# Kernel optimization log

Measured on AMD Instinct MI355X. Metric: run time of the kernel, lower is better.

The kernel has to match this reference:

```python
import jax, jax.numpy as jnp
import numpy as np

B, L, D = 256, 512, 768
ATTN_H, WIDTH_DIM = 1000, 20
BINS = jnp.array([1, 2, 3, 4, 5, 6, 7, 8, 12, 16, 20, 24, 32, 64, 128], dtype=jnp.int64)


def setup_inputs() -> dict:
    key = jax.random.key(0)
    ks = jax.random.split(key, 20)
    s = 0.02
    embeds = jax.random.normal(ks[0], (B, L, D), dtype=jnp.float32)
    spans = jnp.sort(jax.random.randint(ks[1], (B, 2), 0, L, dtype=jnp.int64), axis=1)
    inp = {
        "embeds": embeds,
        "spans": spans,
        # attention scorer: Linear(768,1000) -> LeakyReLU -> Linear(1000,1)
        "aw1": jax.random.normal(ks[2], (D, ATTN_H), dtype=jnp.float32) * s,
        "ab1": jnp.zeros((ATTN_H,), dtype=jnp.float32),
        "aw2": jax.random.normal(ks[3], (ATTN_H, 1), dtype=jnp.float32) * s,
        "ab2": jnp.zeros((1,), dtype=jnp.float32),
        # width embedding: [len(bins)+1 = 16, 20]
        "width_emb": jax.random.normal(ks[4], (16, WIDTH_DIM), dtype=jnp.float32) * s,
        # score MLP: 2324 -> 1024 -> 512 -> 256 -> 30
        "sw1": jax.random.normal(ks[5], (2324, 1024), dtype=jnp.float32) * s,
        "sb1": jnp.zeros((1024,), dtype=jnp.float32),
        "sw2": jax.random.normal(ks[6], (1024, 512), dtype=jnp.float32) * s,
        "sb2": jnp.zeros((512,), dtype=jnp.float32),
        "sw3": jax.random.normal(ks[7], (512, 256), dtype=jnp.float32) * s,
        "sb3": jnp.zeros((256,), dtype=jnp.float32),
        "sw4": jax.random.normal(ks[8], (256, 30), dtype=jnp.float32) * s,
        "sb4": jnp.zeros((30,), dtype=jnp.float32),
    }
    return inp


def reference(embeds, spans, aw1, ab1, aw2, ab2, width_emb,
              sw1, sb1, sw2, sb2, sw3, sb3, sw4, sb4):
    b, l, d = embeds.shape
    start, end = spans[:, 0], spans[:, 1]

    # gather start/end token embeds -> [B, 2*D]
    se = jnp.take_along_axis(embeds, spans[:, :, None], axis=1).reshape(b, 2 * d)

    # attention logits over all tokens: Linear -> LeakyReLU -> Linear
    h = jax.nn.leaky_relu(embeds @ aw1 + ab1)          # [B, L, 1000]
    attns = (h @ aw2 + ab2)[..., 0]                     # [B, L]

    # ragged per-span softmax pooling, vectorized via masking (inclusive span)
    cols = jnp.arange(l, dtype=spans.dtype)[None, :]
    mask = (cols >= start[:, None]) & (cols <= end[:, None])
    w = jax.nn.softmax(jnp.where(mask, attns, jnp.float32(-1e30)), axis=1)
    w = w * mask.astype(w.dtype)
    attn_embeds = jnp.einsum("bl,bld->bd", w, embeds)   # [B, D]

    # width bucket embedding
    widths = end - start + 1
    idx = jnp.sum(widths[:, None] > BINS[None, :], axis=1)
    wemb = width_emb[idx]                                # [B, 20]

    x = jnp.concatenate([se, attn_embeds, wemb], axis=1)  # [B, 2324]
    x = jax.nn.leaky_relu(x @ sw1 + sb1)
    x = jax.nn.leaky_relu(x @ sw2 + sb2)
    x = jax.nn.leaky_relu(x @ sw3 + sb3)
    return x @ sw4 + sb4                                  # [B, 30]
```

## Files before the change

### kernel.cpp

```cpp
#include <hip/hip_runtime.h>
#include <hip/hip_bf16.h>

#define B_   256
#define L_   512
#define D_   768
#define H_   1000
#define NPAD 1024
#define XDIM 2324
#define MAXPOS (B_*L_)

typedef _Float16 half8 __attribute__((ext_vector_type(8)));
typedef float    f32x4 __attribute__((ext_vector_type(4)));

__global__ __launch_bounds__(256) void scan_kernel(const int* __restrict__ spans,
                                                   int* __restrict__ meta) {
    int b = threadIdx.x;
    int s = spans[2 * b], e = spans[2 * b + 1];
    s = min(max(s, 0), L_ - 1);
    e = min(max(e, s), L_ - 1);
    int w = e - s + 1;
    __shared__ int sw[256];
    sw[b] = w;
    __syncthreads();
    for (int d = 1; d < 256; d <<= 1) {
        int v = 0;
        if (b >= d) v = sw[b - d];
        __syncthreads();
        if (b >= d) sw[b] += v;
        __syncthreads();
    }
    meta[b]       = sw[b] - w;
    meta[256 + b] = s;
    meta[512 + b] = e;
    if (b == 255) meta[768] = sw[255];
}

__global__ __launch_bounds__(256) void pos_fill(const int* __restrict__ meta,
                                                int* __restrict__ pos_list) {
    int b = blockIdx.x;
    int off = meta[b], start = meta[256 + b], end = meta[512 + b];
    int w = end - start + 1;
    for (int i = threadIdx.x; i < w; i += blockDim.x)
        pos_list[off + i] = (b << 16) | (start + i);
}

__global__ __launch_bounds__(256) void transpose_w(const float* __restrict__ aw1,
                                                   _Float16* __restrict__ WbT) {
    int k0 = blockIdx.x * 32, n0 = blockIdx.y * 32;
    int tx = threadIdx.x & 31, ty = threadIdx.x >> 5;
    __shared__ float T[32][33];
#pragma unroll
    for (int it = 0; it < 4; it++) {
        int k = k0 + ty + 8 * it;
        int n = n0 + tx;
        T[ty + 8 * it][tx] = (n < H_) ? aw1[(size_t)k * H_ + n] : 0.f;
    }
    __syncthreads();
#pragma unroll
    for (int it = 0; it < 4; it++) {
        int n = n0 + ty + 8 * it;
        WbT[(size_t)n * D_ + k0 + tx] = (_Float16)T[tx][ty + 8 * it];
    }
}

#define AP 776
__global__ __launch_bounds__(256) void attn_gemm_v2(
    const float* __restrict__ embeds, const _Float16* __restrict__ WbT,
    const float* __restrict__ ab1, const float* __restrict__ aw2,
    const int* __restrict__ pos_list, const int* __restrict__ meta,
    float* __restrict__ attns) {
    int npos = meta[768];
    int m0 = blockIdx.x * 32;
    if (m0 >= npos) return;
    int t = threadIdx.x;
    int lane = t & 63, w = t >> 6;
    int q = lane >> 4, l15 = lane & 15;

    __shared__ alignas(16) _Float16 As[32][AP];
    __shared__ unsigned rowoff[32];
    __shared__ float attns_s[4][32];

    if (t < 32) {
        unsigned off = 0;
        int m = m0 + t;
        if (m < npos) {
            int p = pos_list[m];
            off = (unsigned)((p >> 16) * (L_ * D_) + (p & 0xffff) * D_);
        }
        rowoff[t] = off;
    }
    __syncthreads();

    {
        int row = t >> 3;
        int cs = (t & 7) * 96;
        const float* src = embeds + rowoff[row] + cs;
#pragma unroll
        for (int i2 = 0; i2 < 12; i2++) {
            float4 v0 = *(const float4*)(src + i2 * 8);
            float4 v1 = *(const float4*)(src + i2 * 8 + 4);
            half8 h;
            h[0] = (_Float16)v0.x; h[1] = (_Float16)v0.y;
            h[2] = (_Float16)v0.z; h[3] = (_Float16)v0.w;
            h[4] = (_Float16)v1.x; h[5] = (_Float16)v1.y;
            h[6] = (_Float16)v1.z; h[7] = (_Float16)v1.w;
            *(half8*)&As[row][cs + i2 * 8] = h;
        }
    }
    __syncthreads();

    float pacc[2][4];
#pragma unroll
    for (int i = 0; i < 2; i++)
#pragma unroll
        for (int r = 0; r < 4; r++) pacc[i][r] = 0.f;

    for (int g = 0; g < 4; g++) {
        int colbase = w * 256 + g * 64;
        const _Float16* bbase = WbT + (size_t)(colbase + l15) * D_ + q * 8;
        f32x4 acc[2][4];
#pragma unroll
        for (int i = 0; i < 2; i++)
#pragma unroll
            for (int j = 0; j < 4; j++) acc[i][j] = (f32x4){0.f, 0.f, 0.f, 0.f};

        for (int k0 = 0; k0 < D_; k0 += 32) {
            half8 bf[4];
#pragma unroll
            for (int j = 0; j < 4; j++)
                bf[j] = *(const half8*)(bbase + (size_t)j * 16 * D_ + k0);
            half8 af[2];
#pragma unroll
            for (int i = 0; i < 2; i++)
                af[i] = *(const half8*)&As[l15 + 16 * i][k0 + q * 8];
#pragma unroll
            for (int i = 0; i < 2; i++)
#pragma unroll
                for (int j = 0; j < 4; j++)
                    acc[i][j] = __builtin_amdgcn_mfma_f32_16x16x32_f16(af[i], bf[j], acc[i][j], 0, 0, 0);
        }

        float bj[4], aj[4];
#pragma unroll
        for (int j = 0; j < 4; j++) {
            int col = colbase + j * 16 + l15;
            bool v = col < H_;
            bj[j] = v ? ab1[col] : 0.f;
            aj[j] = v ? aw2[col] : 0.f;
        }
#pragma unroll
        for (int i = 0; i < 2; i++) {
#pragma unroll
            for (int r = 0; r < 4; r++) {
                float p = 0.f;
#pragma unroll
                for (int j = 0; j < 4; j++) {
                    float h = acc[i][j][r] + bj[j];
                    h = h > 0.f ? h : 0.01f * h;
                    p += h * aj[j];
                }
                p += __shfl_xor(p, 1);
                p += __shfl_xor(p, 2);
                p += __shfl_xor(p, 4);
                p += __shfl_xor(p, 8);
                pacc[i][r] += p;
            }
        }
    }
    if (l15 == 0) {
#pragma unroll
        for (int i = 0; i < 2; i++)
#pragma unroll
            for (int r = 0; r < 4; r++)
                attns_s[w][i * 16 + q * 4 + r] = pacc[i][r];
    }
    __syncthreads();
    if (t < 32 && m0 + t < npos)
        attns[m0 + t] = attns_s[0][t] + attns_s[1][t] + attns_s[2][t] + attns_s[3][t];
}

__global__ __launch_bounds__(256) void build_x(
    const float* __restrict__ embeds, const float* __restrict__ attns,
    const int* __restrict__ meta, const float* __restrict__ width_emb,
    float* __restrict__ x) {
    int b = blockIdx.x, s = blockIdx.y, t = threadIdx.x;
    int off = meta[b], start = meta[256 + b], end = meta[512 + b];
    int w = end - start + 1;
    __shared__ float sv[512];
    __shared__ float red[256];
    for (int i = t; i < w; i += 256) sv[i] = attns[off + i];
    __syncthreads();
    float m = -3.0e38f;
    for (int i = t; i < w; i += 256) m = fmaxf(m, sv[i]);
    red[t] = m;
    __syncthreads();
    for (int st = 128; st > 0; st >>= 1) {
        if (t < st) red[t] = fmaxf(red[t], red[t + st]);
        __syncthreads();
    }
    float mx = red[0];
    __syncthreads();
    float ssum = 0.f;
    for (int i = t; i < w; i += 256) {
        float e = __expf(sv[i] - mx);
        sv[i] = e;
        ssum += e;
    }
    red[t] = ssum;
    __syncthreads();
    for (int st = 128; st > 0; st >>= 1) {
        if (t < st) red[t] += red[t + st];
        __syncthreads();
    }
    float inv = 1.0f / red[0];
    __syncthreads();

    int dim = s * 256 + t;
    const float* base = embeds + ((size_t)b * L_ + start) * D_ + dim;
    float acc = 0.f;
    int i = 0;
    for (; i + 3 < w; i += 4) {
        float w0 = sv[i], w1 = sv[i + 1], w2 = sv[i + 2], w3 = sv[i + 3];
        const float* p = base + (size_t)i * D_;
        acc += w0 * p[0] + w1 * p[D_] + w2 * p[2 * D_] + w3 * p[3 * D_];
    }
    for (; i < w; i++) acc += sv[i] * base[(size_t)i * D_];

    float* xb = x + (size_t)b * XDIM;
    xb[1536 + dim] = acc * inv;
    xb[dim]        = base[0];
    xb[768 + dim]  = embeds[((size_t)b * L_ + end) * D_ + dim];
    if (s == 0 && t < 20) {
        const int bins[15] = {1, 2, 3, 4, 5, 6, 7, 8, 12, 16, 20, 24, 32, 64, 128};
        int idx = 0;
#pragma unroll
        for (int q2 = 0; q2 < 15; q2++) idx += (w > bins[q2]);
        xb[2304 + t] = width_emb[idx * 20 + t];
    }
}

__global__ __launch_bounds__(256) void mlp_gemm_sk(
    const float* __restrict__ A, const float* __restrict__ W,
    float* __restrict__ out, int M, int N, int K, int kchunk) {
    __shared__ float As[16][68];
    __shared__ float Ws[16][64];
    int t = threadIdx.x;
    int tx = t & 15, ty = t >> 4;
    int m0 = blockIdx.x * 64, n0 = blockIdx.y * 64;
    int ks = blockIdx.z * kchunk;
    int ke = min(ks + kchunk, K);
    if (ks >= ke) return;
    int ar = t >> 2, akc = (t & 3) * 4;
    int wk = t >> 4, wnc = (t & 15) * 4;
    bool n4 = ((N & 3) == 0);

    float acc[4][4];
#pragma unroll
    for (int i = 0; i < 4; i++)
#pragma unroll
        for (int j = 0; j < 4; j++) acc[i][j] = 0.f;

    auto loadA = [&](int k0) -> float4 {
        float4 r = make_float4(0.f, 0.f, 0.f, 0.f);
        int k = k0 + akc;
        if (k < ke) r = *(const float4*)(A + (size_t)(m0 + ar) * K + k);
        return r;
    };
    auto loadW = [&](int k0) -> float4 {
        float4 r = make_float4(0.f, 0.f, 0.f, 0.f);
        int k = k0 + wk;
        if (k < ke) {
            int n = n0 + wnc;
            const float* p = W + (size_t)k * N + n;
            if (n4) {
                r = *(const float4*)p;
            } else {
                float tmp[4];
#pragma unroll
                for (int q2 = 0; q2 < 4; q2++)
                    tmp[q2] = (n + q2 < N) ? p[q2] : 0.f;
                r = make_float4(tmp[0], tmp[1], tmp[2], tmp[3]);
            }
        }
        return r;
    };

    float4 aR = loadA(ks), wR = loadW(ks);
    for (int k0 = ks; k0 < ke; k0 += 16) {
        As[akc + 0][ar] = aR.x;
        As[akc + 1][ar] = aR.y;
        As[akc + 2][ar] = aR.z;
        As[akc + 3][ar] = aR.w;
        *(float4*)&Ws[wk][wnc] = wR;
        __syncthreads();
        if (k0 + 16 < ke) { aR = loadA(k0 + 16); wR = loadW(k0 + 16); }
#pragma unroll
        for (int kk = 0; kk < 16; kk++) {
            float4 a = *(const float4*)&As[kk][ty * 4];
            float4 b = *(const float4*)&Ws[kk][tx * 4];
            float av[4] = {a.x, a.y, a.z, a.w};
            float bv[4] = {b.x, b.y, b.z, b.w};
#pragma unroll
            for (int i = 0; i < 4; i++)
#pragma unroll
                for (int j = 0; j < 4; j++) acc[i][j] += av[i] * bv[j];
        }
        __syncthreads();
    }
#pragma unroll
    for (int i = 0; i < 4; i++) {
#pragma unroll
        for (int j = 0; j < 4; j++) {
            int nn = n0 + tx * 4 + j;
            if (nn < N)
                atomicAdd(&out[(size_t)(m0 + ty * 4 + i) * N + nn], acc[i][j]);
        }
    }
}

__global__ __launch_bounds__(256) void bias_act(
    const float* __restrict__ src, const float* __restrict__ bias,
    float* __restrict__ dst, int total, int N, int leaky) {
    int i = blockIdx.x * 256 + threadIdx.x;
    int stride = gridDim.x * 256;
    for (; i < total; i += stride) {
        float v = src[i] + bias[i % N];
        if (leaky) v = v > 0.f ? v : 0.01f * v;
        dst[i] = v;
    }
}

extern "C" void kernel_launch(void* const* d_in, const int* in_sizes, int n_in,
                              void* d_out, int out_size, void* d_ws, size_t ws_size,
                              hipStream_t stream) {
    const float* embeds    = (const float*)d_in[0];
    const int*   spans     = (const int*)d_in[1];
    const float* aw1       = (const float*)d_in[2];
    const float* ab1       = (const float*)d_in[3];
    const float* aw2       = (const float*)d_in[4];
    const float* width_emb = (const float*)d_in[6];
    const float* sw1 = (const float*)d_in[7],  *sb1 = (const float*)d_in[8];
    const float* sw2 = (const float*)d_in[9],  *sb2 = (const float*)d_in[10];
    const float* sw3 = (const float*)d_in[11], *sb3 = (const float*)d_in[12];
    const float* sw4 = (const float*)d_in[13], *sb4 = (const float*)d_in[14];
    float* out = (float*)d_out;

    char* ws = (char*)d_ws;
    float*     attns    = (float*)ws;
    int*       pos_list = (int*)(ws + (size_t)MAXPOS * 4);
    int*       meta     = (int*)(ws + (size_t)MAXPOS * 8);
    _Float16*  WbT      = (_Float16*)(ws + (size_t)MAXPOS * 8 + 4096);
    float* x  = (float*)(ws + (size_t)MAXPOS * 8 + 4096 + (size_t)NPAD * D_ * 2);
    float* y1 = x + (size_t)B_ * XDIM;
    float* y2 = y1 + (size_t)B_ * 1024;
    float* y3 = y2 + (size_t)B_ * 512;
    float* y4 = y3 + (size_t)B_ * 256;
    size_t ybytes = ((size_t)B_ * (1024 + 512 + 256 + 30)) * 4;

    hipMemsetAsync(y1, 0, ybytes, stream);
    scan_kernel<<<1, 256, 0, stream>>>(spans, meta);
    pos_fill<<<B_, 256, 0, stream>>>(meta, pos_list);
    transpose_w<<<dim3(D_ / 32, NPAD / 32), 256, 0, stream>>>(aw1, WbT);
    attn_gemm_v2<<<MAXPOS / 32, 256, 0, stream>>>(
        embeds, WbT, ab1, aw2, pos_list, meta, attns);
    build_x<<<dim3(B_, 3), 256, 0, stream>>>(embeds, attns, meta, width_emb, x);

    mlp_gemm_sk<<<dim3(4, 16, 8), 256, 0, stream>>>(x,  sw1, y1, B_, 1024, XDIM, 292);
    bias_act<<<256, 256, 0, stream>>>(y1, sb1, y1, B_ * 1024, 1024, 1);
    mlp_gemm_sk<<<dim3(4, 8, 8), 256, 0, stream>>>(y1, sw2, y2, B_, 512, 1024, 128);
    bias_act<<<128, 256, 0, stream>>>(y2, sb2, y2, B_ * 512, 512, 1);
    mlp_gemm_sk<<<dim3(4, 4, 8), 256, 0, stream>>>(y2, sw3, y3, B_, 256, 512, 64);
    bias_act<<<64, 256, 0, stream>>>(y3, sb3, y3, B_ * 256, 256, 1);
    mlp_gemm_sk<<<dim3(4, 1, 8), 256, 0, stream>>>(y3, sw4, y4, B_, 30, 256, 32);
    bias_act<<<30, 256, 0, stream>>>(y4, sb4, out, B_ * 30, 30, 0);
}
```

Measured before the change: 903.7 us.

## Pre-pack attention weights into MFMA fragment layout and double-buffer B loads

Replaces the weight transpose with a packing kernel that writes aw1 in the exact per-lane MFMA fragment order, so each wave's B loads become fully contiguous 16-byte-per-lane reads. The attention GEMM inner loop now double-buffers the B fragments across k-chunks to overlap global loads with MFMA work. The span pooling loop is unrolled to eight independent accumulators to raise memory-level parallelism. The packing kernel's reads of aw1 are strided and uncoalesced, which may cost more than the old transpose, and the extra accumulators slightly change floating-point summation order.

Result: slower. 937.1 us (+3.7%).

```diff
diff --git a/kernel.cpp b/kernel.cpp
--- a/kernel.cpp
+++ b/kernel.cpp
@@ -8,6 +8,7 @@
 #define NPAD 1024
 #define XDIM 2324
 #define MAXPOS (B_*L_)
+#define NKC  24
 
 typedef _Float16 half8 __attribute__((ext_vector_type(8)));
 typedef float    f32x4 __attribute__((ext_vector_type(4)));
@@ -44,28 +45,24 @@
         pos_list[off + i] = (b << 16) | (start + i);
 }
 
-__global__ __launch_bounds__(256) void transpose_w(const float* __restrict__ aw1,
-                                                   _Float16* __restrict__ WbT) {
-    int k0 = blockIdx.x * 32, n0 = blockIdx.y * 32;
-    int tx = threadIdx.x & 31, ty = threadIdx.x >> 5;
-    __shared__ float T[32][33];
-#pragma unroll
-    for (int it = 0; it < 4; it++) {
-        int k = k0 + ty + 8 * it;
-        int n = n0 + tx;
-        T[ty + 8 * it][tx] = (n < H_) ? aw1[(size_t)k * H_ + n] : 0.f;
-    }
-    __syncthreads();
-#pragma unroll
-    for (int it = 0; it < 4; it++) {
-        int n = n0 + ty + 8 * it;
-        WbT[(size_t)n * D_ + k0 + tx] = (_Float16)T[tx][ty + 8 * it];
-    }
+__global__ __launch_bounds__(64) void pack_b(const float* __restrict__ aw1,
+                                             _Float16* __restrict__ Bp) {
+    int gi = blockIdx.x, kc = blockIdx.y;
+    int l = threadIdx.x;
+    int col = gi * 16 + (l & 15);
+    int kbase = kc * 32 + (l >> 4) * 8;
+    half8 h;
+#pragma unroll
+    for (int e = 0; e < 8; e++) {
+        float v = (col < H_) ? aw1[(size_t)(kbase + e) * H_ + col] : 0.f;
+        h[e] = (_Float16)v;
+    }
+    *(half8*)&Bp[(((size_t)gi * NKC + kc) * 64 + l) * 8] = h;
 }
 
 #define AP 776
 __global__ __launch_bounds__(256) void attn_gemm_v2(
-    const float* __restrict__ embeds, const _Float16* __restrict__ WbT,
+    const float* __restrict__ embeds, const _Float16* __restrict__ Bp,
     const float* __restrict__ ab1, const float* __restrict__ aw2,
     const int* __restrict__ pos_list, const int* __restrict__ meta,
     float* __restrict__ attns) {
@@ -117,27 +114,50 @@
 
     for (int g = 0; g < 4; g++) {
         int colbase = w * 256 + g * 64;
-        const _Float16* bbase = WbT + (size_t)(colbase + l15) * D_ + q * 8;
+        int gi0 = colbase >> 4;
+        const _Float16* bb = Bp + ((size_t)gi0 * NKC * 64) * 8 + (size_t)lane * 8;
         f32x4 acc[2][4];
 #pragma unroll
         for (int i = 0; i < 2; i++)
 #pragma unroll
             for (int j = 0; j < 4; j++) acc[i][j] = (f32x4){0.f, 0.f, 0.f, 0.f};
 
-        for (int k0 = 0; k0 < D_; k0 += 32) {
-            half8 bf[4];
+        half8 bfA[4], bfB[4];
+#pragma unroll
+        for (int j = 0; j < 4; j++)
+            bfA[j] = *(const half8*)(bb + (size_t)j * (NKC * 64 * 8));
+
+        for (int kc = 0; kc < NKC; kc += 2) {
 #pragma unroll
             for (int j = 0; j < 4; j++)
-                bf[j] = *(const half8*)(bbase + (size_t)j * 16 * D_ + k0);
-            half8 af[2];
-#pragma unroll
-            for (int i = 0; i < 2; i++)
-                af[i] = *(const half8*)&As[l15 + 16 * i][k0 + q * 8];
-#pragma unroll
-            for (int i = 0; i < 2; i++)
+                bfB[j] = *(const half8*)(bb + (size_t)j * (NKC * 64 * 8) + (size_t)(kc + 1) * 512);
+            {
+                half8 af[2];
+#pragma unroll
+                for (int i = 0; i < 2; i++)
+                    af[i] = *(const half8*)&As[l15 + 16 * i][kc * 32 + q * 8];
+#pragma unroll
+                for (int i = 0; i < 2; i++)
+#pragma unroll
+                    for (int j = 0; j < 4; j++)
+                        acc[i][j] = __builtin_amdgcn_mfma_f32_16x16x32_f16(af[i], bfA[j], acc[i][j], 0, 0, 0);
+            }
+            if (kc + 2 < NKC) {
 #pragma unroll
                 for (int j = 0; j < 4; j++)
-                    acc[i][j] = __builtin_amdgcn_mfma_f32_16x16x32_f16(af[i], bf[j], acc[i][j], 0, 0, 0);
+                    bfA[j] = *(const half8*)(bb + (size_t)j * (NKC * 64 * 8) + (size_t)(kc + 2) * 512);
+            }
+            {
+                half8 af[2];
+#pragma unroll
+                for (int i = 0; i < 2; i++)
+                    af[i] = *(const half8*)&As[l15 + 16 * i][(kc + 1) * 32 + q * 8];
+#pragma unroll
+                for (int i = 0; i < 2; i++)
+#pragma unroll
+                    for (int j = 0; j < 4; j++)
+                        acc[i][j] = __builtin_amdgcn_mfma_f32_16x16x32_f16(af[i], bfB[j], acc[i][j], 0, 0, 0);
+            }
         }
 
         float bj[4], aj[4];
@@ -217,14 +237,22 @@
 
     int dim = s * 256 + t;
     const float* base = embeds + ((size_t)b * L_ + start) * D_ + dim;
-    float acc = 0.f;
+    float a0 = 0.f, a1 = 0.f, a2 = 0.f, a3 = 0.f;
+    float a4 = 0.f, a5 = 0.f, a6 = 0.f, a7 = 0.f;
     int i = 0;
-    for (; i + 3 < w; i += 4) {
-        float w0 = sv[i], w1 = sv[i + 1], w2 = sv[i + 2], w3 = sv[i + 3];
+    for (; i + 8 <= w; i += 8) {
         const float* p = base + (size_t)i * D_;
-        acc += w0 * p[0] + w1 * p[D_] + w2 * p[2 * D_] + w3 * p[3 * D_];
-    }
-    for (; i < w; i++) acc += sv[i] * base[(size_t)i * D_];
+        a0 += sv[i]     * p[0];
+        a1 += sv[i + 1] * p[D_];
+        a2 += sv[i + 2] * p[2 * D_];
+        a3 += sv[i + 3] * p[3 * D_];
+        a4 += sv[i + 4] * p[4 * D_];
+        a5 += sv[i + 5] * p[5 * D_];
+        a6 += sv[i + 6] * p[6 * D_];
+        a7 += sv[i + 7] * p[7 * D_];
+    }
+    for (; i < w; i++) a0 += sv[i] * base[(size_t)i * D_];
+    float acc = ((a0 + a1) + (a2 + a3)) + ((a4 + a5) + (a6 + a7));
 
     float* xb = x + (size_t)b * XDIM;
     xb[1536 + dim] = acc * inv;
@@ -349,7 +377,7 @@
     float*     attns    = (float*)ws;
     int*       pos_list = (int*)(ws + (size_t)MAXPOS * 4);
     int*       meta     = (int*)(ws + (size_t)MAXPOS * 8);
-    _Float16*  WbT      = (_Float16*)(ws + (size_t)MAXPOS * 8 + 4096);
+    _Float16*  Bp       = (_Float16*)(ws + (size_t)MAXPOS * 8 + 4096);
     float* x  = (float*)(ws + (size_t)MAXPOS * 8 + 4096 + (size_t)NPAD * D_ * 2);
     float* y1 = x + (size_t)B_ * XDIM;
     float* y2 = y1 + (size_t)B_ * 1024;
@@ -360,9 +388,9 @@
     hipMemsetAsync(y1, 0, ybytes, stream);
     scan_kernel<<<1, 256, 0, stream>>>(spans, meta);
     pos_fill<<<B_, 256, 0, stream>>>(meta, pos_list);
-    transpose_w<<<dim3(D_ / 32, NPAD / 32), 256, 0, stream>>>(aw1, WbT);
+    pack_b<<<dim3(NPAD / 16, NKC), 64, 0, stream>>>(aw1, Bp);
     attn_gemm_v2<<<MAXPOS / 32, 256, 0, stream>>>(
-        embeds, WbT, ab1, aw2, pos_list, meta, attns);
+        embeds, Bp, ab1, aw2, pos_list, meta, attns);
     build_x<<<dim3(B_, 3), 256, 0, stream>>>(embeds, attns, meta, width_emb, x);
 
     mlp_gemm_sk<<<dim3(4, 16, 8), 256, 0, stream>>>(x,  sw1, y1, B_, 1024, XDIM, 292);
```
